# Kernel tuning notes

Measured on AMD Instinct MI355X. Metric: run time of the kernel, lower is better.

The kernel has to match this reference:

```python
import jax, jax.numpy as jnp
import numpy as np

B, T, CIN, H, COUT, OUT_T = 512, 128, 64, 256, 64, 32


def setup_inputs() -> dict:
    key = jax.random.key(0)
    ks = jax.random.split(key, 12)
    s = lambda fan: 1.0 / np.sqrt(fan)
    return {
        "times": jnp.arange(T, dtype=jnp.float32),
        "coeffs": jax.random.normal(ks[0], (B, T, CIN), jnp.float32),
        "noise": jax.random.normal(ks[1], (T - 1, B, H), jnp.float32),
        # initial_network: Linear(input_channels, hidden_channels)
        "W_init": jax.random.normal(ks[2], (CIN, H), jnp.float32) * s(CIN),
        "b_init": jax.random.normal(ks[3], (H,), jnp.float32) * s(CIN),
        # SDE func drift / diffusion (diagonal noise)
        "Wf": jax.random.normal(ks[4], (H, H), jnp.float32) * s(H),
        "bf": jax.random.normal(ks[5], (H,), jnp.float32) * s(H),
        "Wg": jax.random.normal(ks[6], (H, H), jnp.float32) * s(H),
        "bg": jax.random.normal(ks[7], (H,), jnp.float32) * s(H),
        # head: Linear(H,H) -> ReLU -> Linear(H,COUT)
        "W1": jax.random.normal(ks[8], (H, H), jnp.float32) * s(H),
        "b1": jax.random.normal(ks[9], (H,), jnp.float32) * s(H),
        "W2": jax.random.normal(ks[10], (H, COUT), jnp.float32) * s(H),
        "b2": jax.random.normal(ks[11], (COUT,), jnp.float32) * s(H),
        "output_time": OUT_T,
    }


def reference(times, coeffs, noise, W_init, b_init, Wf, bf, Wg, bg, W1, b1, W2, b2, output_time):
    # dt = max(min(diff(times)), 0.001) as in the torch module
    dt = jnp.maximum(jnp.min(times[1:] - times[:-1]), 0.001)
    sqrt_dt = jnp.sqrt(dt)

    # z0 = initial_network(X.evaluate(times[0])) -> first control value
    x0 = coeffs[:, 0, :]                       # [B, CIN]
    z0 = x0 @ W_init + b_init                  # [B, H]

    def step(z, eps):
        f = jnp.tanh(z @ Wf + bf)              # drift
        g = jax.nn.sigmoid(z @ Wg + bg)        # diagonal diffusion
        z_next = z + f * dt + g * (sqrt_dt * eps)
        return z_next, z_next

    _, zs = jax.lax.scan(step, z0, noise)      # [T-1, B, H]
    z_t = jnp.concatenate([z0[None], zs], 0)   # [T, B, H]
    z_t = jnp.swapaxes(z_t, 0, 1)              # [B, T, H]  (transpose(0,1))

    h = z_t[:, z_t.shape[1] - output_time:, :] # [B, output_time, H]
    pred_y = jax.nn.relu(h @ W1 + b1) @ W2 + b2
    return pred_y
```

## Files before the change

### kernel.cpp

```cpp
#include <hip/hip_runtime.h>
#include <hip/hip_fp8.h>
#include <math.h>

#define B_      512
#define T_      128
#define CIN_    64
#define H_      256
#define COUT_   64
#define OUT_T_  32
#define NB_     16
#define NSTEP_  (T_ - 1)
#define HWIN_   (T_ - OUT_T_)
#define CUT_    32

#define INV16_  1.52587890625e-5f

typedef _Float16 half8  __attribute__((ext_vector_type(8)));
typedef float    floatx4 __attribute__((ext_vector_type(4)));
typedef long     longx2 __attribute__((ext_vector_type(2)));

#define LDS_TOTAL_ 152072

#define BARRIER_LGKM() asm volatile("s_waitcnt lgkmcnt(0)\n\ts_barrier" ::: "memory")

__device__ __forceinline__ float tanh_fast(float x){
  float e = __expf(2.0f * x);
  return 1.0f - 2.0f * __builtin_amdgcn_rcpf(e + 1.0f);
}
__device__ __forceinline__ float sigm_fast(float x){
  return __builtin_amdgcn_rcpf(1.0f + __expf(-x));
}
__device__ __forceinline__ int SWZ16(int r){ return ((r >> 2) & 3) << 4; }
__device__ __forceinline__ int SWZ8 (int r){ return ((r >> 2) & 3) << 5; }

__global__ void packFG_kernel(const float* __restrict__ W, _Float16* __restrict__ Ph,
                              unsigned char* __restrict__ P8){
  int i = blockIdx.x * blockDim.x + threadIdx.x;
  if (i >= H_ * H_) return;
  int k = i >> 8, n = i & 255;
  float w = W[i];
  _Float16 h = (_Float16)w;
  int off16 = (((n >> 5) * 16 + (k >> 5) * 2 + ((n >> 4) & 1)) << 10)
            + ((((k >> 3) & 3) * 16 + (n & 15)) << 4) + ((k & 7) << 1);
  *(_Float16*)((char*)Ph + off16) = h;
  int lanei = ((k >> 3) & 3) * 16 + (n & 15);
  int off8 = ((n >> 5) << 13) + ((k >> 5) << 10) + (lanei << 4)
           + (((n >> 4) & 1) << 3) + (k & 7);
  P8[off8] = __hip_cvt_float_to_fp8((w - (float)h) * 65536.0f,
                                    __HIP_SATFINITE, __HIP_E4M3);
}

__global__ void pack_kernel(const float* __restrict__ W, _Float16* __restrict__ Ph,
                            int K, int N){
  int i = blockIdx.x * blockDim.x + threadIdx.x;
  if (i >= K * N) return;
  int k = i / N, n = i - k * N;
  Ph[((k >> 5) * N + n) * 32 + (k & 31)] = (_Float16)W[i];
}

__global__ __launch_bounds__(512, 2) void scan_kernel(
    const float* __restrict__ times,
    const float* __restrict__ coeffs,
    const float* __restrict__ noise,
    const float* __restrict__ W_init,
    const float* __restrict__ b_init,
    const float* __restrict__ bf,
    const float* __restrict__ bg,
    const _Float16* __restrict__ WfPh,
    const _Float16* __restrict__ WgPh,
    const unsigned char* __restrict__ W8lF,
    const unsigned char* __restrict__ W8lG,
    _Float16* __restrict__ zhist)
{
  extern __shared__ __align__(16) char dynlds[];
  unsigned char* w8lds = (unsigned char*)dynlds;
  _Float16* zst   = (_Float16*)(dynlds + 131072);
  _Float16* zlt   = (_Float16*)(dynlds + 139264);
  unsigned char* z8t = (unsigned char*)(dynlds + 147456);
  float* diffs = (float*)(dynlds + 151552);
  float* dtsh  = (float*)(dynlds + 152064);
  float* x0_lds = (float*)(dynlds);
  float* z0f    = (float*)(dynlds + 4096);

  const int tid  = threadIdx.x;
  const int lane = tid & 63;
  const int wv   = tid >> 6;
  const int lo   = lane & 15;
  const int hi   = lane >> 4;
  const int b0   = blockIdx.x * NB_;

  if (tid < 127) diffs[tid] = times[tid + 1] - times[tid];
  if (tid == 127) diffs[127] = 3.4e38f;

  float bfv[2], bgv[2];
  #pragma unroll
  for (int t2 = 0; t2 < 2; ++t2){
    bfv[t2] = bf[32*wv + 16*t2 + lo];
    bgv[t2] = bg[32*wv + 16*t2 + lo];
  }

  for (int i = tid; i < NB_ * CIN_; i += 512)
    x0_lds[i] = coeffs[(size_t)(b0 + (i >> 6)) * (T_ * CIN_) + (i & 63)];
  __syncthreads();

  if (tid < 64){
    float m = fminf(diffs[tid], diffs[tid + 64]);
    #pragma unroll
    for (int o = 32; o; o >>= 1) m = fminf(m, __shfl_down(m, o, 64));
    if (tid == 0){
      float dt0 = fmaxf(m, 0.001f);
      dtsh[0] = dt0; dtsh[1] = sqrtf(dt0);
    }
  }

  {
    int r = tid & 15, c0 = (tid >> 4) * 8;
    float acc[8];
    #pragma unroll
    for (int j = 0; j < 8; ++j) acc[j] = b_init[c0 + j];
    for (int k = 0; k < CIN_; ++k){
      float x = x0_lds[r * CIN_ + k];
      const float* wrow = W_init + k * H_ + c0;
      #pragma unroll
      for (int j = 0; j < 8; ++j) acc[j] += x * wrow[j];
    }
    #pragma unroll
    for (int j = 0; j < 8; ++j) z0f[r * H_ + c0 + j] = acc[j];
  }
  __syncthreads();

  const float dt = dtsh[0], sqdt = dtsh[1];

  float zreg[2][4];
  #pragma unroll
  for (int t2 = 0; t2 < 2; ++t2){
    int col = 32*wv + 16*t2 + lo;
    #pragma unroll
    for (int rg = 0; rg < 4; ++rg)
      zreg[t2][rg] = z0f[(hi*4 + rg) * H_ + col];
  }
  for (int i = tid; i < NB_ * H_; i += 512){
    int rr = i >> 8;
    float zv = z0f[i];
    _Float16 zh = (_Float16)zv;
    int idx = i ^ SWZ16(rr);
    zst[idx] = zh;
    zlt[idx] = (_Float16)(zv - (float)zh);
    z8t[i ^ SWZ8(rr)] = __hip_cvt_float_to_fp8(zv, __HIP_SATFINITE, __HIP_E4M3);
  }
  __syncthreads();

  for (int i = tid * 16; i < 65536; i += 512 * 16){
    *(int4*)(w8lds + i)         = *(const int4*)(W8lF + i);
    *(int4*)(w8lds + 65536 + i) = *(const int4*)(W8lG + i);
  }
  __syncthreads();

  const int eb0 = (b0 + hi*4) * H_ + 32*wv + lo;
  const size_t zh0 = (size_t)(b0 + hi*4) * (OUT_T_ * H_) + 32*wv + lo;

  const int wb16 = (wv << 14) + (((hi << 4) + lo) << 4);
  const char* pfB = (const char*)WfPh + wb16;
  const char* pgB = (const char*)WgPh + wb16;
  const int w8b = (wv << 13) + (lane << 4);

  int aoff[8], a8off[8];
  #pragma unroll
  for (int kt = 0; kt < 8; ++kt){
    aoff[kt]  = (lo*H_ + kt*32 + hi*8) ^ SWZ16(lo);
    a8off[kt] = (lo*H_ + kt*32 + hi*8) ^ SWZ8(lo);
  }
  int woff[2][4], w8off_[2][4];
  #pragma unroll
  for (int t2 = 0; t2 < 2; ++t2)
    #pragma unroll
    for (int rg = 0; rg < 4; ++rg){
      int row = hi*4 + rg, col = 32*wv + 16*t2 + lo;
      woff[t2][rg]   = (row * H_ + col) ^ SWZ16(row);
      w8off_[t2][rg] = (row * H_ + col) ^ SWZ8(row);
    }

  floatx4 uF[2], uG[2], u8F[2], u8G[2];
  uF[0] = (floatx4){0.f,0.f,0.f,0.f}; uF[1] = uF[0];
  uG[0] = uF[0]; uG[1] = uF[0];
  u8F[0] = uF[0]; u8F[1] = uF[0]; u8G[0] = uF[0]; u8G[1] = uF[0];
  #pragma unroll
  for (int kt = 0; kt < 8; ++kt){
    half8 ah = *(const half8*)&zst[aoff[kt]];
    half8 al = *(const half8*)&zlt[aoff[kt]];
    long  a8 = *(const long*)&z8t[a8off[kt]];
    longx2 wf8 = *(const longx2*)(w8lds + w8b + (kt << 10));
    longx2 wg8 = *(const longx2*)(w8lds + 65536 + w8b + (kt << 10));
    #pragma unroll
    for (int t2 = 0; t2 < 2; ++t2){
      half8 whf = *(const half8*)(pfB + (kt*2 + t2)*1024);
      half8 whg = *(const half8*)(pgB + (kt*2 + t2)*1024);
      uF[t2]  = __builtin_amdgcn_mfma_f32_16x16x32_f16(ah, whf, uF[t2], 0,0,0);
      uF[t2]  = __builtin_amdgcn_mfma_f32_16x16x32_f16(al, whf, uF[t2], 0,0,0);
      uG[t2]  = __builtin_amdgcn_mfma_f32_16x16x32_f16(ah, whg, uG[t2], 0,0,0);
      uG[t2]  = __builtin_amdgcn_mfma_f32_16x16x32_f16(al, whg, uG[t2], 0,0,0);
      u8F[t2] = __builtin_amdgcn_mfma_f32_16x16x32_fp8_fp8(a8, wf8[t2], u8F[t2], 0,0,0);
      u8G[t2] = __builtin_amdgcn_mfma_f32_16x16x32_fp8_fp8(a8, wg8[t2], u8G[t2], 0,0,0);
    }
  }
  #pragma unroll
  for (int t2 = 0; t2 < 2; ++t2)
    #pragma unroll
    for (int rg = 0; rg < 4; ++rg){
      uF[t2][rg] += bfv[t2];
      uG[t2][rg] += bgv[t2];
    }

  const char* epp = (const char*)(noise + eb0);
  float eps[2][4];
  #pragma unroll
  for (int t2 = 0; t2 < 2; ++t2)
    #pragma unroll
    for (int rg = 0; rg < 4; ++rg)
      eps[t2][rg] = *(const float*)(epp + (rg*H_ + t2*16)*4);

  __syncthreads();

  unsigned int wlo = 0;

  for (int s = 0; s < CUT_; ++s){
    const char* pf = pfB + wlo;
    const char* pg = pgB + wlo;

    #pragma unroll
    for (int t2 = 0; t2 < 2; ++t2){
      float dzv[4];
      #pragma unroll
      for (int rg = 0; rg < 4; ++rg){
        float uf = fmaf(INV16_, u8F[t2][rg], uF[t2][rg]);
        float ug = fmaf(INV16_, u8G[t2][rg], uG[t2][rg]);
        float f = tanh_fast(uf);
        float g = sigm_fast(ug);
        float dz = fmaf(g, sqdt * eps[t2][rg], f * dt);
        dzv[rg] = dz;
        zreg[t2][rg] += dz;
        _Float16 dh = (_Float16)dz;
        zst[woff[t2][rg]] = dh;
        zlt[woff[t2][rg]] = (_Float16)(dz - (float)dh);
      }
      int p01 = __builtin_amdgcn_cvt_pk_fp8_f32(dzv[0], dzv[1], 0, false);
      int p23 = __builtin_amdgcn_cvt_pk_fp8_f32(dzv[2], dzv[3], 0, false);
      z8t[w8off_[t2][0]] = (unsigned char)(p01);
      z8t[w8off_[t2][1]] = (unsigned char)(p01 >> 8);
      z8t[w8off_[t2][2]] = (unsigned char)(p23);
      z8t[w8off_[t2][3]] = (unsigned char)(p23 >> 8);
    }

    epp += (size_t)B_ * H_ * 4;
    #pragma unroll
    for (int t2 = 0; t2 < 2; ++t2)
      #pragma unroll
      for (int rg = 0; rg < 4; ++rg)
        eps[t2][rg] = *(const float*)(epp + (rg*H_ + t2*16)*4);
    half8 whf[2][2], whg[2][2];
    #pragma unroll
    for (int kt = 0; kt < 2; ++kt)
      #pragma unroll
      for (int t2 = 0; t2 < 2; ++t2){
        whf[kt][t2] = *(const half8*)(pf + (kt*2 + t2)*1024);
        whg[kt][t2] = *(const half8*)(pg + (kt*2 + t2)*1024);
      }

    BARRIER_LGKM();

    #pragma unroll
    for (int kt = 0; kt < 8; ++kt){
      half8 ah = *(const half8*)&zst[aoff[kt]];
      half8 al = *(const half8*)&zlt[aoff[kt]];
      long  a8 = *(const long*)&z8t[a8off[kt]];
      longx2 wf8 = *(const longx2*)(w8lds + w8b + (kt << 10));
      longx2 wg8 = *(const longx2*)(w8lds + 65536 + w8b + (kt << 10));
      half8 f0 = whf[kt & 1][0], f1 = whf[kt & 1][1];
      half8 g0 = whg[kt & 1][0], g1 = whg[kt & 1][1];
      if (kt + 2 < 8){
        #pragma unroll
        for (int t2 = 0; t2 < 2; ++t2){
          whf[kt & 1][t2] = *(const half8*)(pf + ((kt+2)*2 + t2)*1024);
          whg[kt & 1][t2] = *(const half8*)(pg + ((kt+2)*2 + t2)*1024);
        }
      }
      uF[0]  = __builtin_amdgcn_mfma_f32_16x16x32_f16(ah, f0, uF[0], 0,0,0);
      uF[1]  = __builtin_amdgcn_mfma_f32_16x16x32_f16(ah, f1, uF[1], 0,0,0);
      uG[0]  = __builtin_amdgcn_mfma_f32_16x16x32_f16(ah, g0, uG[0], 0,0,0);
      uG[1]  = __builtin_amdgcn_mfma_f32_16x16x32_f16(ah, g1, uG[1], 0,0,0);
      uF[0]  = __builtin_amdgcn_mfma_f32_16x16x32_f16(al, f0, uF[0], 0,0,0);
      uF[1]  = __builtin_amdgcn_mfma_f32_16x16x32_f16(al, f1, uF[1], 0,0,0);
      uG[0]  = __builtin_amdgcn_mfma_f32_16x16x32_f16(al, g0, uG[0], 0,0,0);
      uG[1]  = __builtin_amdgcn_mfma_f32_16x16x32_f16(al, g1, uG[1], 0,0,0);
      u8F[0] = __builtin_amdgcn_mfma_f32_16x16x32_fp8_fp8(a8, wf8[0], u8F[0], 0,0,0);
      u8F[1] = __builtin_amdgcn_mfma_f32_16x16x32_fp8_fp8(a8, wf8[1], u8F[1], 0,0,0);
      u8G[0] = __builtin_amdgcn_mfma_f32_16x16x32_fp8_fp8(a8, wg8[0], u8G[0], 0,0,0);
      u8G[1] = __builtin_amdgcn_mfma_f32_16x16x32_fp8_fp8(a8, wg8[1], u8G[1], 0,0,0);
    }

    BARRIER_LGKM();
    asm volatile("" : "+v"(wlo));
  }

  for (int s = CUT_; s < NSTEP_; ++s){
    _Float16* zw = (s & 1) ? zlt : zst;
    const char* pf = pfB + wlo;
    const char* pg = pgB + wlo;

    #pragma unroll
    for (int t2 = 0; t2 < 2; ++t2)
      #pragma unroll
      for (int rg = 0; rg < 4; ++rg){
        float uf = fmaf(INV16_, u8F[t2][rg], uF[t2][rg]);
        float ug = fmaf(INV16_, u8G[t2][rg], uG[t2][rg]);
        float f = tanh_fast(uf);
        float g = sigm_fast(ug);
        float dz = fmaf(g, sqdt * eps[t2][rg], f * dt);
        zreg[t2][rg] += dz;
        zw[woff[t2][rg]] = (_Float16)dz;
      }

    if (s >= HWIN_ - 1){
      int sl = s - (HWIN_ - 1);
      #pragma unroll
      for (int t2 = 0; t2 < 2; ++t2)
        #pragma unroll
        for (int rg = 0; rg < 4; ++rg)
          zhist[zh0 + (size_t)rg*(OUT_T_*H_) + sl*H_ + t2*16] = (_Float16)zreg[t2][rg];
    }

    half8 whf[4][2], whg[4][2];
    if (s + 1 < NSTEP_){
      epp += (size_t)B_ * H_ * 4;
      #pragma unroll
      for (int t2 = 0; t2 < 2; ++t2)
        #pragma unroll
        for (int rg = 0; rg < 4; ++rg)
          eps[t2][rg] = *(const float*)(epp + (rg*H_ + t2*16)*4);
      #pragma unroll
      for (int kt = 0; kt < 4; ++kt)
        #pragma unroll
        for (int t2 = 0; t2 < 2; ++t2){
          whf[kt][t2] = *(const half8*)(pf + (kt*2 + t2)*1024);
          whg[kt][t2] = *(const half8*)(pg + (kt*2 + t2)*1024);
        }
    }

    BARRIER_LGKM();

    if (s + 1 < NSTEP_){
      #pragma unroll
      for (int kt = 0; kt < 8; ++kt){
        half8 ah = *(const half8*)&zw[aoff[kt]];
        half8 f0 = whf[kt & 3][0], f1 = whf[kt & 3][1];
        half8 g0 = whg[kt & 3][0], g1 = whg[kt & 3][1];
        if (kt + 4 < 8){
          #pragma unroll
          for (int t2 = 0; t2 < 2; ++t2){
            whf[kt & 3][t2] = *(const half8*)(pf + ((kt+4)*2 + t2)*1024);
            whg[kt & 3][t2] = *(const half8*)(pg + ((kt+4)*2 + t2)*1024);
          }
        }
        uF[0] = __builtin_amdgcn_mfma_f32_16x16x32_f16(ah, f0, uF[0], 0,0,0);
        uF[1] = __builtin_amdgcn_mfma_f32_16x16x32_f16(ah, f1, uF[1], 0,0,0);
        uG[0] = __builtin_amdgcn_mfma_f32_16x16x32_f16(ah, g0, uG[0], 0,0,0);
        uG[1] = __builtin_amdgcn_mfma_f32_16x16x32_f16(ah, g1, uG[1], 0,0,0);
      }
    }
    asm volatile("" : "+v"(wlo));
  }
}

__global__ __launch_bounds__(256) void head_kernel(
    const _Float16* __restrict__ zhist,
    const _Float16* __restrict__ W1P,
    const _Float16* __restrict__ W2P,
    const float* __restrict__ b1,
    const float* __restrict__ b2,
    float* __restrict__ out)
{
  __shared__ __align__(16) _Float16 hbuf[64 * H_];
  __shared__ __align__(16) _Float16 ubuf[64 * H_];

  const int tid  = threadIdx.x;
  const int lane = tid & 63;
  const int wv   = tid >> 6;
  const int lo   = lane & 15;
  const int hi   = lane >> 4;
  const int m0   = blockIdx.x * 64;

  for (int c = tid; c < 64 * 32; c += 256){
    int rr = c >> 5, c8 = (c & 31) * 8;
    *(half8*)&hbuf[(rr * H_ + c8) ^ ((rr & 7) << 3)] =
        *(const half8*)&zhist[(size_t)(m0 + rr) * H_ + c8];
  }

  half8 w1f[4][8];
  #pragma unroll
  for (int nt = 0; nt < 4; ++nt){
    int n0 = 64*wv + 16*nt + lo;
    #pragma unroll
    for (int kt = 0; kt < 8; ++kt)
      w1f[nt][kt] = *(const half8*)(W1P + (kt*H_ + n0)*32 + 8*hi);
  }
  half8 w2f[8];
  #pragma unroll
  for (int kt = 0; kt < 8; ++kt)
    w2f[kt] = *(const half8*)(W2P + (kt*COUT_ + 16*wv + lo)*32 + 8*hi);

  float b1v[4];
  #pragma unroll
  for (int nt = 0; nt < 4; ++nt) b1v[nt] = b1[64*wv + 16*nt + lo];
  float b2v = b2[16*wv + lo];

  __syncthreads();

  for (int mt = 0; mt < 4; ++mt){
    half8 a[8];
    #pragma unroll
    for (int kt = 0; kt < 8; ++kt)
      a[kt] = *(const half8*)&hbuf[((mt*16 + lo) * H_ + kt*32 + hi*8) ^ ((lo & 7) << 3)];
    #pragma unroll
    for (int nt = 0; nt < 4; ++nt){
      floatx4 acc = {0.f,0.f,0.f,0.f};
      #pragma unroll
      for (int kt = 0; kt < 8; ++kt)
        acc = __builtin_amdgcn_mfma_f32_16x16x32_f16(a[kt], w1f[nt][kt], acc, 0,0,0);
      #pragma unroll
      for (int rg = 0; rg < 4; ++rg){
        float u = fmaxf(acc[rg] + b1v[nt], 0.0f);
        int rr = mt*16 + hi*4 + rg;
        int cc = 64*wv + 16*nt + lo;
        ubuf[(rr * H_ + cc) ^ ((rr & 7) << 3)] = (_Float16)u;
      }
    }
  }
  __syncthreads();

  for (int mt = 0; mt < 4; ++mt){
    half8 a[8];
    #pragma unroll
    for (int kt = 0; kt < 8; ++kt)
      a[kt] = *(const half8*)&ubuf[((mt*16 + lo) * H_ + kt*32 + hi*8) ^ ((lo & 7) << 3)];
    floatx4 acc = {0.f,0.f,0.f,0.f};
    #pragma unroll
    for (int kt = 0; kt < 8; ++kt)
      acc = __builtin_amdgcn_mfma_f32_16x16x32_f16(a[kt], w2f[kt], acc, 0,0,0);
    #pragma unroll
    for (int rg = 0; rg < 4; ++rg)
      out[(size_t)(m0 + mt*16 + hi*4 + rg) * COUT_ + 16*wv + lo] = acc[rg] + b2v;
  }
}

extern "C" void kernel_launch(void* const* d_in, const int* in_sizes, int n_in,
                              void* d_out, int out_size, void* d_ws, size_t ws_size,
                              hipStream_t stream) {
  const float* times  = (const float*)d_in[0];
  const float* coeffs = (const float*)d_in[1];
  const float* noise  = (const float*)d_in[2];
  const float* W_init = (const float*)d_in[3];
  const float* b_init = (const float*)d_in[4];
  const float* Wf     = (const float*)d_in[5];
  const float* bf     = (const float*)d_in[6];
  const float* Wg     = (const float*)d_in[7];
  const float* bg     = (const float*)d_in[8];
  const float* W1     = (const float*)d_in[9];
  const float* b1     = (const float*)d_in[10];
  const float* W2     = (const float*)d_in[11];
  const float* b2     = (const float*)d_in[12];

  char* ws = (char*)d_ws;
  _Float16*      zhist = (_Float16*)(ws);
  _Float16*      WfPh  = (_Float16*)(ws + 8388608);
  _Float16*      WgPh  = (_Float16*)(ws + 8519680);
  unsigned char* W8lF  = (unsigned char*)(ws + 8650752);
  unsigned char* W8lG  = (unsigned char*)(ws + 8716288);
  _Float16*      W1Ph  = (_Float16*)(ws + 8781824);
  _Float16*      W2Ph  = (_Float16*)(ws + 8978432);

  packFG_kernel<<<(H_*H_ + 255)/256, 256, 0, stream>>>(Wf, WfPh, W8lF);
  packFG_kernel<<<(H_*H_ + 255)/256, 256, 0, stream>>>(Wg, WgPh, W8lG);
  pack_kernel<<<(H_*H_ + 255)/256, 256, 0, stream>>>(W1, W1Ph, H_, H_);
  pack_kernel<<<(H_*COUT_ + 255)/256, 256, 0, stream>>>(W2, W2Ph, H_, COUT_);

  hipFuncSetAttribute((const void*)scan_kernel,
                      hipFuncAttributeMaxDynamicSharedMemorySize, LDS_TOTAL_);
  scan_kernel<<<B_ / NB_, 512, LDS_TOTAL_, stream>>>(
      times, coeffs, noise, W_init, b_init, bf, bg,
      WfPh, WgPh, W8lF, W8lG, zhist);

  head_kernel<<<(B_ * OUT_T_) / 64, 256, 0, stream>>>(zhist, W1Ph, W2Ph, b1, b2,
                                                      (float*)d_out);
}
```

Baseline: 388.6 us.

## Double-buffer z state in LDS and stream FP8 G weights from global

Moves the FP8 diffusion weights out of LDS so they are loaded from global/L2 with register prefetching. This frees LDS space for double-buffered z hi/lo/fp8 tiles. With ping-pong buffers, the second barrier per step in the first phase is removed. It also shrinks LDS, which may allow more occupancy. The cost is extra global/L2 traffic for the FP8 G weights on every step. Because the later loop's buffer mapping changed, it depends on the parity of the first-phase writes staying consistent.

```diff
diff --git a/kernel.cpp b/kernel.cpp
--- a/kernel.cpp
+++ b/kernel.cpp
@@ -19,7 +19,7 @@
 typedef float    floatx4 __attribute__((ext_vector_type(4)));
 typedef long     longx2 __attribute__((ext_vector_type(2)));
 
-#define LDS_TOTAL_ 152072
+#define LDS_TOTAL_ 107016
 
 #define BARRIER_LGKM() asm volatile("s_waitcnt lgkmcnt(0)\n\ts_barrier" ::: "memory")
 
@@ -74,11 +74,14 @@
 {
   extern __shared__ __align__(16) char dynlds[];
   unsigned char* w8lds = (unsigned char*)dynlds;
-  _Float16* zst   = (_Float16*)(dynlds + 131072);
-  _Float16* zlt   = (_Float16*)(dynlds + 139264);
-  unsigned char* z8t = (unsigned char*)(dynlds + 147456);
-  float* diffs = (float*)(dynlds + 151552);
-  float* dtsh  = (float*)(dynlds + 152064);
+  _Float16* zstb0 = (_Float16*)(dynlds + 65536);
+  _Float16* zstb1 = (_Float16*)(dynlds + 73728);
+  _Float16* zltb0 = (_Float16*)(dynlds + 81920);
+  _Float16* zltb1 = (_Float16*)(dynlds + 90112);
+  unsigned char* z8b0 = (unsigned char*)(dynlds + 98304);
+  unsigned char* z8b1 = (unsigned char*)(dynlds + 102400);
+  float* diffs = (float*)(dynlds + 106496);
+  float* dtsh  = (float*)(dynlds + 107008);
   float* x0_lds = (float*)(dynlds);
   float* z0f    = (float*)(dynlds + 4096);
 
@@ -144,16 +147,14 @@
     float zv = z0f[i];
     _Float16 zh = (_Float16)zv;
     int idx = i ^ SWZ16(rr);
-    zst[idx] = zh;
-    zlt[idx] = (_Float16)(zv - (float)zh);
-    z8t[i ^ SWZ8(rr)] = __hip_cvt_float_to_fp8(zv, __HIP_SATFINITE, __HIP_E4M3);
-  }
-  __syncthreads();
-
-  for (int i = tid * 16; i < 65536; i += 512 * 16){
-    *(int4*)(w8lds + i)         = *(const int4*)(W8lF + i);
-    *(int4*)(w8lds + 65536 + i) = *(const int4*)(W8lG + i);
-  }
+    zstb0[idx] = zh;
+    zltb0[idx] = (_Float16)(zv - (float)zh);
+    z8b0[i ^ SWZ8(rr)] = __hip_cvt_float_to_fp8(zv, __HIP_SATFINITE, __HIP_E4M3);
+  }
+  __syncthreads();
+
+  for (int i = tid * 16; i < 65536; i += 512 * 16)
+    *(int4*)(w8lds + i) = *(const int4*)(W8lF + i);
   __syncthreads();
 
   const int eb0 = (b0 + hi*4) * H_ + 32*wv + lo;
@@ -163,6 +164,7 @@
   const char* pfB = (const char*)WfPh + wb16;
   const char* pgB = (const char*)WgPh + wb16;
   const int w8b = (wv << 13) + (lane << 4);
+  const char* p8gB = (const char*)W8lG + w8b;
 
   int aoff[8], a8off[8];
   #pragma unroll
@@ -186,11 +188,11 @@
   u8F[0] = uF[0]; u8F[1] = uF[0]; u8G[0] = uF[0]; u8G[1] = uF[0];
   #pragma unroll
   for (int kt = 0; kt < 8; ++kt){
-    half8 ah = *(const half8*)&zst[aoff[kt]];
-    half8 al = *(const half8*)&zlt[aoff[kt]];
-    long  a8 = *(const long*)&z8t[a8off[kt]];
+    half8 ah = *(const half8*)&zstb0[aoff[kt]];
+    half8 al = *(const half8*)&zltb0[aoff[kt]];
+    long  a8 = *(const long*)&z8b0[a8off[kt]];
     longx2 wf8 = *(const longx2*)(w8lds + w8b + (kt << 10));
-    longx2 wg8 = *(const longx2*)(w8lds + 65536 + w8b + (kt << 10));
+    longx2 wg8 = *(const longx2*)(p8gB + (kt << 10));
     #pragma unroll
     for (int t2 = 0; t2 < 2; ++t2){
       half8 whf = *(const half8*)(pfB + (kt*2 + t2)*1024);
@@ -224,8 +226,12 @@
   unsigned int wlo = 0;
 
   for (int s = 0; s < CUT_; ++s){
-    const char* pf = pfB + wlo;
-    const char* pg = pgB + wlo;
+    _Float16* zstw = (s & 1) ? zstb1 : zstb0;
+    _Float16* zltw = (s & 1) ? zltb1 : zltb0;
+    unsigned char* z8w = (s & 1) ? z8b1 : z8b0;
+    const char* pf  = pfB  + wlo;
+    const char* pg  = pgB  + wlo;
+    const char* p8g = p8gB + wlo;
 
     #pragma unroll
     for (int t2 = 0; t2 < 2; ++t2){
@@ -240,15 +246,15 @@
         dzv[rg] = dz;
         zreg[t2][rg] += dz;
         _Float16 dh = (_Float16)dz;
-        zst[woff[t2][rg]] = dh;
-        zlt[woff[t2][rg]] = (_Float16)(dz - (float)dh);
+        zstw[woff[t2][rg]] = dh;
+        zltw[woff[t2][rg]] = (_Float16)(dz - (float)dh);
       }
       int p01 = __builtin_amdgcn_cvt_pk_fp8_f32(dzv[0], dzv[1], 0, false);
       int p23 = __builtin_amdgcn_cvt_pk_fp8_f32(dzv[2], dzv[3], 0, false);
-      z8t[w8off_[t2][0]] = (unsigned char)(p01);
-      z8t[w8off_[t2][1]] = (unsigned char)(p01 >> 8);
-      z8t[w8off_[t2][2]] = (unsigned char)(p23);
-      z8t[w8off_[t2][3]] = (unsigned char)(p23 >> 8);
+      z8w[w8off_[t2][0]] = (unsigned char)(p01);
+      z8w[w8off_[t2][1]] = (unsigned char)(p01 >> 8);
+      z8w[w8off_[t2][2]] = (unsigned char)(p23);
+      z8w[w8off_[t2][3]] = (unsigned char)(p23 >> 8);
     }
 
     epp += (size_t)B_ * H_ * 4;
@@ -258,23 +264,26 @@
       for (int rg = 0; rg < 4; ++rg)
         eps[t2][rg] = *(const float*)(epp + (rg*H_ + t2*16)*4);
     half8 whf[2][2], whg[2][2];
-    #pragma unroll
-    for (int kt = 0; kt < 2; ++kt)
+    longx2 wg8p[2];
+    #pragma unroll
+    for (int kt = 0; kt < 2; ++kt){
       #pragma unroll
       for (int t2 = 0; t2 < 2; ++t2){
         whf[kt][t2] = *(const half8*)(pf + (kt*2 + t2)*1024);
         whg[kt][t2] = *(const half8*)(pg + (kt*2 + t2)*1024);
       }
+      wg8p[kt] = *(const longx2*)(p8g + (kt << 10));
+    }
 
     BARRIER_LGKM();
 
     #pragma unroll
     for (int kt = 0; kt < 8; ++kt){
-      half8 ah = *(const half8*)&zst[aoff[kt]];
-      half8 al = *(const half8*)&zlt[aoff[kt]];
-      long  a8 = *(const long*)&z8t[a8off[kt]];
+      half8 ah = *(const half8*)&zstw[aoff[kt]];
+      half8 al = *(const half8*)&zltw[aoff[kt]];
+      long  a8 = *(const long*)&z8w[a8off[kt]];
       longx2 wf8 = *(const longx2*)(w8lds + w8b + (kt << 10));
-      longx2 wg8 = *(const longx2*)(w8lds + 65536 + w8b + (kt << 10));
+      longx2 wg8 = wg8p[kt & 1];
       half8 f0 = whf[kt & 1][0], f1 = whf[kt & 1][1];
       half8 g0 = whg[kt & 1][0], g1 = whg[kt & 1][1];
       if (kt + 2 < 8){
@@ -283,6 +292,7 @@
           whf[kt & 1][t2] = *(const half8*)(pf + ((kt+2)*2 + t2)*1024);
           whg[kt & 1][t2] = *(const half8*)(pg + ((kt+2)*2 + t2)*1024);
         }
+        wg8p[kt & 1] = *(const longx2*)(p8g + ((kt+2) << 10));
       }
       uF[0]  = __builtin_amdgcn_mfma_f32_16x16x32_f16(ah, f0, uF[0], 0,0,0);
       uF[1]  = __builtin_amdgcn_mfma_f32_16x16x32_f16(ah, f1, uF[1], 0,0,0);
@@ -297,13 +307,11 @@
       u8G[0] = __builtin_amdgcn_mfma_f32_16x16x32_fp8_fp8(a8, wg8[0], u8G[0], 0,0,0);
       u8G[1] = __builtin_amdgcn_mfma_f32_16x16x32_fp8_fp8(a8, wg8[1], u8G[1], 0,0,0);
     }
-
-    BARRIER_LGKM();
     asm volatile("" : "+v"(wlo));
   }
 
   for (int s = CUT_; s < NSTEP_; ++s){
-    _Float16* zw = (s & 1) ? zlt : zst;
+    _Float16* zw = (s & 1) ? zstb1 : zstb0;
     const char* pf = pfB + wlo;
     const char* pg = pgB + wlo;
 
```

New measurement: 399.0 us. 2.7% more time.
